# Kernel optimization log

Hardware: AMD Instinct MI355X
Metric: run time of the kernel (lower is better)

The kernel has to match this reference:

```python
import jax, jax.numpy as jnp
import numpy as np

B, T, D = 2, 2048, 1024
NH, DH = 16, 64  # inner = NH*DH = D
SCALE_INIT = 0.02


def setup_inputs() -> dict:
    key = jax.random.key(0)
    kx, kq, kk, kv, ko = jax.random.split(key, 5)
    return {
        "x": jax.random.normal(kx, (B, T, D), dtype=jnp.float32),
        "Wq": jax.random.normal(kq, (D, NH * DH), dtype=jnp.float32) * SCALE_INIT,
        "Wk": jax.random.normal(kk, (D, NH * DH), dtype=jnp.float32) * SCALE_INIT,
        "Wv": jax.random.normal(kv, (D, NH * DH), dtype=jnp.float32) * SCALE_INIT,
        "Wo": jax.random.normal(ko, (NH * DH, D), dtype=jnp.float32) * SCALE_INIT,
    }


def reference(x, Wq, Wk, Wv, Wo):
    # x: (B, T, D)
    b, t, _ = x.shape

    def split_heads(h):
        # (B, T, NH*DH) -> (B, NH, T, DH)
        return h.reshape(b, t, NH, DH).transpose(0, 2, 1, 3)

    q = split_heads(x @ Wq)
    k = split_heads(x @ Wk)
    v = split_heads(x @ Wv)

    scale = jnp.asarray(1.0 / np.sqrt(DH), dtype=x.dtype)
    # The per-chunk loop in the original is mathematically equivalent to
    # full causal attention: each query row attends to keys with k_pos <= q_pos.
    scores = jnp.einsum("bhqd,bhkd->bhqk", q, k) * scale  # (B, NH, T, T)
    causal_mask = jnp.arange(t)[None, :] > jnp.arange(t)[:, None]  # k_pos > q_pos
    scores = jnp.where(causal_mask, -jnp.inf, scores)
    attn = jax.nn.softmax(scores, axis=-1)
    attn = jnp.nan_to_num(attn)  # matches torch.nan_to_num (no fully-masked rows in causal case)
    o = jnp.einsum("bhqk,bhkd->bhqd", attn, v)  # (B, NH, T, DH)
    o = o.transpose(0, 2, 1, 3).reshape(b, t, NH * DH)  # merge heads
    return o @ Wo  # (B, T, D)
```

## Files before the change

### kernel.cpp

```cpp
#include <hip/hip_runtime.h>

#define Bsz 2
#define Tsz 2048
#define Dsz 1024
#define NHsz 16
#define Msz (Bsz*Tsz)

typedef unsigned short bfu;
typedef __attribute__((ext_vector_type(8))) short short8;
typedef __attribute__((ext_vector_type(4))) short short4v;
typedef __attribute__((ext_vector_type(4))) float floatx4;

__device__ __forceinline__ bfu f2bf(float f) {
  unsigned int u = __builtin_bit_cast(unsigned int, f);
  u += 0x7fffu + ((u >> 16) & 1u);
  return (bfu)(u >> 16);
}

__device__ __forceinline__ void async16(const void* g, void* l) {
  void* gnc = (void*)g;
  __builtin_amdgcn_global_load_lds((__attribute__((address_space(1))) void*)gnc,
                                   (__attribute__((address_space(3))) void*)l,
                                   16, 0, 0);
}

__global__ __launch_bounds__(256) void convert_x(const float* __restrict__ x,
                                                 bfu* __restrict__ xb) {
  int i = blockIdx.x * 256 + threadIdx.x;
  float4 v = ((const float4*)x)[i];
  short4v o;
  o[0] = (short)f2bf(v.x); o[1] = (short)f2bf(v.y);
  o[2] = (short)f2bf(v.z); o[3] = (short)f2bf(v.w);
  *(short4v*)(xb + (size_t)i * 4) = o;
}

__global__ __launch_bounds__(256) void transpose_w(const float* __restrict__ W0, const float* __restrict__ W1,
                                                   const float* __restrict__ W2, const float* __restrict__ W3,
                                                   bfu* __restrict__ wt) {
  __shared__ float tile[32][33];
  const float* W = blockIdx.z == 0 ? W0 : blockIdx.z == 1 ? W1 : blockIdx.z == 2 ? W2 : W3;
  bfu* WT = wt + (size_t)blockIdx.z * Dsz * Dsz;
  int tx = threadIdx.x, ty = threadIdx.y;
  int kb = blockIdx.y * 32, nb = blockIdx.x * 32;
#pragma unroll
  for (int i = 0; i < 4; ++i)
    tile[ty + i*8][tx] = W[(size_t)(kb + ty + i*8) * Dsz + nb + tx];
  __syncthreads();
#pragma unroll
  for (int i = 0; i < 4; ++i)
    WT[(size_t)(nb + ty + i*8) * Dsz + kb + tx] = f2bf(tile[tx][ty + i*8]);
}

template <bool F32OUT>
__global__ __launch_bounds__(256) void gemm128(const bfu* __restrict__ A, const bfu* __restrict__ Bt0,
                                               void* __restrict__ C0, int K, int N,
                                               size_t strideB, size_t strideC, float scale0) {
  const int tid = threadIdx.x, wave = tid >> 6, lane = tid & 63;
  const int g = lane >> 4, c = lane & 15;
  const int m0 = blockIdx.y * 128, n0 = blockIdx.x * 128;
  const bfu* Bt = Bt0 + strideB * blockIdx.z;
  const float scale = (blockIdx.z == 0) ? scale0 : 1.0f;
  __shared__ bfu As[128 * 32];
  __shared__ bfu Bs[128 * 32];
  floatx4 acc[4][4] = {};
  const int srow = lane >> 2, scol = (lane & 3) * 8;
  const bfu* gA = A  + (size_t)(m0 + srow) * K + scol;
  const bfu* gB = Bt + (size_t)(n0 + srow) * K + scol;
  const int wm = (wave >> 1) * 64, wn = (wave & 1) * 64;
  for (int k0 = 0; k0 < K; k0 += 32) {
    __syncthreads();
#pragma unroll
    for (int cc = 0; cc < 2; ++cc) {
      const int chunk = wave * 2 + cc;
      async16(gA + (size_t)chunk * 16 * K + k0, &As[chunk * 512]);
      async16(gB + (size_t)chunk * 16 * K + k0, &Bs[chunk * 512]);
    }
    __syncthreads();
    short8 afr[4], bfr[4];
#pragma unroll
    for (int t = 0; t < 4; ++t) afr[t] = *(const short8*)&As[(wm + t*16 + c) * 32 + g * 8];
#pragma unroll
    for (int t = 0; t < 4; ++t) bfr[t] = *(const short8*)&Bs[(wn + t*16 + c) * 32 + g * 8];
#pragma unroll
    for (int i = 0; i < 4; ++i)
#pragma unroll
      for (int j = 0; j < 4; ++j)
        acc[i][j] = __builtin_amdgcn_mfma_f32_16x16x32_bf16(afr[i], bfr[j], acc[i][j], 0, 0, 0);
  }
  const bool vtrans = (!F32OUT) && (blockIdx.z == 2);
#pragma unroll
  for (int i = 0; i < 4; ++i) {
#pragma unroll
    for (int j = 0; j < 4; ++j) {
      const int m = m0 + wm + i*16 + g*4;
      const int n = n0 + wn + j*16 + c;
      if (vtrans) {
        bfu* vtp = (bfu*)C0 + (size_t)2 * strideC;
        size_t o = ((size_t)((m >> 11) * 16 + (n >> 6)) * 64 + (n & 63)) * Tsz + (m & 2047);
        short4v pk;
#pragma unroll
        for (int r = 0; r < 4; ++r) pk[r] = (short)f2bf(acc[i][j][r]);
        *(short4v*)&vtp[o] = pk;
      } else {
#pragma unroll
        for (int r = 0; r < 4; ++r) {
          float v = acc[i][j][r] * scale;
          if (F32OUT) ((float*)C0)[(size_t)(m + r) * N + n] = v;
          else        ((bfu*)C0)[strideC * blockIdx.z + (size_t)(m + r) * N + n] = f2bf(v);
        }
      }
    }
  }
}

__global__ __launch_bounds__(256, 2) void attn_kernel(const bfu* __restrict__ qkv,
                                                      bfu* __restrict__ obuf) {
  const int tid = threadIdx.x, wave = tid >> 6, lane = tid & 63;
  const int g = (lane >> 4) & 3, c = lane & 15, c7 = c & 7;
  const int bh = blockIdx.y, b = bh >> 4, h = bh & 15;
  const size_t hb = (size_t)b * Tsz * Dsz + h * 64;
  const bfu* Qp = qkv + hb;
  const bfu* Kp = qkv + (size_t)Msz * Dsz + hb;
  const bfu* Vt = qkv + (size_t)2 * Msz * Dsz + (size_t)bh * 64 * Tsz;

  __shared__ bfu Ks[128 * 64];
  __shared__ bfu Vs[64 * 128];
  __shared__ bfu Ps[4][16 * 128];

  const int kst_row = lane >> 3;
  const int kst_off = ((lane & 7) ^ kst_row) << 3;
  const int vst_row = lane >> 4;

  for (int half = 0; half < 2; ++half) {
    const int j = half ? (31 - (int)blockIdx.x) : (int)blockIdx.x;
    const int qw = j * 64 + wave * 16;
    const int ktm = j >> 1;

    short8 bq[2];
#pragma unroll
    for (int kk = 0; kk < 2; ++kk)
      bq[kk] = *(const short8*)(Qp + (size_t)(qw + c) * Dsz + kk * 32 + g * 8);

    floatx4 acc[4] = {};
    float mi = -3.0e38f, li = 0.0f;

    for (int kt = 0; kt <= ktm; ++kt) {
      __syncthreads();
#pragma unroll
      for (int cc = 0; cc < 4; ++cc) {
        const int ch = wave * 4 + cc;
        async16(Kp + (size_t)(kt * 128 + ch * 8 + kst_row) * Dsz + kst_off, &Ks[ch * 512]);
        const int drow = ch * 4 + vst_row;
        async16(Vt + (size_t)drow * Tsz + kt * 128 + (((lane & 15) ^ (drow & 7)) << 3), &Vs[ch * 512]);
      }
      __syncthreads();

      floatx4 st[8] = {};
#pragma unroll
      for (int kk = 0; kk < 2; ++kk)
#pragma unroll
        for (int mk = 0; mk < 8; ++mk) {
          const short8 kf = *(const short8*)&Ks[(mk * 16 + c) * 64 + (((kk * 4 + g) ^ c7) << 3)];
          st[mk] = __builtin_amdgcn_mfma_f32_16x16x32_bf16(kf, bq[kk], st[mk], 0, 0, 0);
        }

      if (kt == ktm) {
#pragma unroll
        for (int mk = 0; mk < 8; ++mk) {
          const int keyb = kt * 128 + mk * 16 + g * 4;
#pragma unroll
          for (int r = 0; r < 4; ++r)
            if (keyb + r > qw + c) st[mk][r] = -1.0e38f;
        }
      }

      float mloc = -3.0e38f;
#pragma unroll
      for (int mk = 0; mk < 8; ++mk)
#pragma unroll
        for (int r = 0; r < 4; ++r) mloc = fmaxf(mloc, st[mk][r]);
      mloc = fmaxf(mloc, __shfl_xor(mloc, 16));
      mloc = fmaxf(mloc, __shfl_xor(mloc, 32));
      const float mnew = fmaxf(mi, mloc);
      const float alpha = exp2f(mi - mnew);
      mi = mnew;
      float sum = 0.0f;
#pragma unroll
      for (int mk = 0; mk < 8; ++mk) {
        short4v pk;
#pragma unroll
        for (int r = 0; r < 4; ++r) {
          const float p = exp2f(st[mk][r] - mnew);
          sum += p;
          pk[r] = (short)f2bf(p);
        }
        *(short4v*)&Ps[wave][c * 128 + (((mk * 2 + (g >> 1)) ^ c7) << 3) + ((g & 1) << 2)] = pk;
      }
      sum += __shfl_xor(sum, 16);
      sum += __shfl_xor(sum, 32);
      li = li * alpha + sum;

      float al[4];
#pragma unroll
      for (int r = 0; r < 4; ++r) al[r] = __shfl(alpha, (lane & 48) | (g * 4 + r));
#pragma unroll
      for (int nd = 0; nd < 4; ++nd)
#pragma unroll
        for (int r = 0; r < 4; ++r) acc[nd][r] *= al[r];

#pragma unroll
      for (int kc = 0; kc < 4; ++kc) {
        const int sl = ((kc * 4 + g) ^ c7) << 3;
        const short8 pf = *(const short8*)&Ps[wave][c * 128 + sl];
#pragma unroll
        for (int nd = 0; nd < 4; ++nd) {
          const short8 vf = *(const short8*)&Vs[(nd * 16 + c) * 128 + sl];
          acc[nd] = __builtin_amdgcn_mfma_f32_16x16x32_bf16(pf, vf, acc[nd], 0, 0, 0);
        }
      }
    }

    float inv[4];
#pragma unroll
    for (int r = 0; r < 4; ++r) inv[r] = 1.0f / __shfl(li, (lane & 48) | (g * 4 + r));
#pragma unroll
    for (int nd = 0; nd < 4; ++nd)
#pragma unroll
      for (int r = 0; r < 4; ++r)
        obuf[(size_t)(b * Tsz + qw + g * 4 + r) * Dsz + h * 64 + nd * 16 + c] =
            f2bf(acc[nd][r] * inv[r]);
  }
}

extern "C" void kernel_launch(void* const* d_in, const int* in_sizes, int n_in,
                              void* d_out, int out_size, void* d_ws, size_t ws_size,
                              hipStream_t stream) {
  const float* x  = (const float*)d_in[0];
  const float* Wq = (const float*)d_in[1];
  const float* Wk = (const float*)d_in[2];
  const float* Wv = (const float*)d_in[3];
  const float* Wo = (const float*)d_in[4];
  float* out = (float*)d_out;

  bfu* xb   = (bfu*)d_ws;
  bfu* wt   = xb  + (size_t)Msz * Dsz;
  bfu* qkv  = wt  + (size_t)4 * Dsz * Dsz;
  bfu* obuf = qkv + (size_t)3 * Msz * Dsz;

  convert_x<<<dim3(Msz * Dsz / (256 * 4)), dim3(256), 0, stream>>>(x, xb);
  transpose_w<<<dim3(32, 32, 4), dim3(32, 8), 0, stream>>>(Wq, Wk, Wv, Wo, wt);
  gemm128<false><<<dim3(Dsz / 128, Msz / 128, 3), dim3(256), 0, stream>>>(
      xb, wt, (void*)qkv, Dsz, Dsz, (size_t)Dsz * Dsz, (size_t)Msz * Dsz,
      0.125f * 1.44269504088896f);
  attn_kernel<<<dim3(16, Bsz * NHsz), dim3(256), 0, stream>>>(qkv, obuf);
  gemm128<true><<<dim3(Dsz / 128, Msz / 128, 1), dim3(256), 0, stream>>>(
      obuf, wt + (size_t)3 * Dsz * Dsz, (void*)out, Dsz, Dsz, (size_t)0, (size_t)0, 1.0f);
}
```

Before: 206.4 us.

## Fuse x conversion into QKV GEMM and register-prefetch attention K/V tiles

Removes the separate convert_x kernel: the QKV GEMM now reads fp32 x directly, converts it to bf16 in registers and prefetches the next A tile while computing. The attention kernel swaps its async global-to-LDS K/V loads for register prefetch of the next tile, stored to LDS at the top of each iteration. bf16 packing now uses the HIP intrinsic conversions in place of manual rounding. Together these drop one launch and the xb round trip and aim to overlap loads with compute. The cost is more register pressure and double fp32 A traffic, since the three z-slices each re-read x.

Result: slower. 210.9 us (+2.1%).

```diff
diff --git a/kernel.cpp b/kernel.cpp
--- a/kernel.cpp
+++ b/kernel.cpp
@@ -1,4 +1,6 @@
 #include <hip/hip_runtime.h>
+#include <hip/hip_bf16.h>
+#include <string.h>
 
 #define Bsz 2
 #define Tsz 2048
@@ -17,21 +19,31 @@
   return (bfu)(u >> 16);
 }
 
+__device__ __forceinline__ short4v pack4bf(float a, float b, float c_, float d) {
+  __hip_bfloat162 h01 = __float22bfloat162_rn(make_float2(a, b));
+  __hip_bfloat162 h23 = __float22bfloat162_rn(make_float2(c_, d));
+  uint2 uu;
+  memcpy(&uu.x, &h01, 4);
+  memcpy(&uu.y, &h23, 4);
+  return __builtin_bit_cast(short4v, uu);
+}
+
+__device__ __forceinline__ short8 pack8bf(float4 a, float4 b) {
+  __hip_bfloat162 h0 = __float22bfloat162_rn(make_float2(a.x, a.y));
+  __hip_bfloat162 h1 = __float22bfloat162_rn(make_float2(a.z, a.w));
+  __hip_bfloat162 h2 = __float22bfloat162_rn(make_float2(b.x, b.y));
+  __hip_bfloat162 h3 = __float22bfloat162_rn(make_float2(b.z, b.w));
+  uint4 u;
+  memcpy(&u.x, &h0, 4); memcpy(&u.y, &h1, 4);
+  memcpy(&u.z, &h2, 4); memcpy(&u.w, &h3, 4);
+  return __builtin_bit_cast(short8, u);
+}
+
 __device__ __forceinline__ void async16(const void* g, void* l) {
   void* gnc = (void*)g;
   __builtin_amdgcn_global_load_lds((__attribute__((address_space(1))) void*)gnc,
                                    (__attribute__((address_space(3))) void*)l,
                                    16, 0, 0);
-}
-
-__global__ __launch_bounds__(256) void convert_x(const float* __restrict__ x,
-                                                 bfu* __restrict__ xb) {
-  int i = blockIdx.x * 256 + threadIdx.x;
-  float4 v = ((const float4*)x)[i];
-  short4v o;
-  o[0] = (short)f2bf(v.x); o[1] = (short)f2bf(v.y);
-  o[2] = (short)f2bf(v.z); o[3] = (short)f2bf(v.w);
-  *(short4v*)(xb + (size_t)i * 4) = o;
 }
 
 __global__ __launch_bounds__(256) void transpose_w(const float* __restrict__ W0, const float* __restrict__ W1,
@@ -51,8 +63,8 @@
     WT[(size_t)(nb + ty + i*8) * Dsz + kb + tx] = f2bf(tile[tx][ty + i*8]);
 }
 
-template <bool F32OUT>
-__global__ __launch_bounds__(256) void gemm128(const bfu* __restrict__ A, const bfu* __restrict__ Bt0,
+template <bool F32OUT, bool AF32>
+__global__ __launch_bounds__(256) void gemm128(const void* __restrict__ Ain, const bfu* __restrict__ Bt0,
                                                void* __restrict__ C0, int K, int N,
                                                size_t strideB, size_t strideC, float scale0) {
   const int tid = threadIdx.x, wave = tid >> 6, lane = tid & 63;
@@ -64,18 +76,38 @@
   __shared__ bfu Bs[128 * 32];
   floatx4 acc[4][4] = {};
   const int srow = lane >> 2, scol = (lane & 3) * 8;
-  const bfu* gA = A  + (size_t)(m0 + srow) * K + scol;
   const bfu* gB = Bt + (size_t)(n0 + srow) * K + scol;
   const int wm = (wave >> 1) * 64, wn = (wave & 1) * 64;
+
+  short8 areg[2];
+  if (AF32) {
+#pragma unroll
+    for (int cc = 0; cc < 2; ++cc) {
+      const float* pa = (const float*)Ain +
+          (size_t)(m0 + (wave*2 + cc)*16 + srow) * K + scol;
+      areg[cc] = pack8bf(((const float4*)pa)[0], ((const float4*)pa)[1]);
+    }
+  }
+  const bfu* gA = AF32 ? nullptr : (const bfu*)Ain + (size_t)(m0 + srow) * K + scol;
+
   for (int k0 = 0; k0 < K; k0 += 32) {
     __syncthreads();
 #pragma unroll
     for (int cc = 0; cc < 2; ++cc) {
       const int chunk = wave * 2 + cc;
-      async16(gA + (size_t)chunk * 16 * K + k0, &As[chunk * 512]);
+      if (AF32) *(short8*)&As[chunk * 512 + lane * 8] = areg[cc];
+      else      async16(gA + (size_t)chunk * 16 * K + k0, &As[chunk * 512]);
       async16(gB + (size_t)chunk * 16 * K + k0, &Bs[chunk * 512]);
     }
     __syncthreads();
+    if (AF32 && k0 + 32 < K) {
+#pragma unroll
+      for (int cc = 0; cc < 2; ++cc) {
+        const float* pa = (const float*)Ain +
+            (size_t)(m0 + (wave*2 + cc)*16 + srow) * K + (k0 + 32) + scol;
+        areg[cc] = pack8bf(((const float4*)pa)[0], ((const float4*)pa)[1]);
+      }
+    }
     short8 afr[4], bfr[4];
 #pragma unroll
     for (int t = 0; t < 4; ++t) afr[t] = *(const short8*)&As[(wm + t*16 + c) * 32 + g * 8];
@@ -97,10 +129,7 @@
       if (vtrans) {
         bfu* vtp = (bfu*)C0 + (size_t)2 * strideC;
         size_t o = ((size_t)((m >> 11) * 16 + (n >> 6)) * 64 + (n & 63)) * Tsz + (m & 2047);
-        short4v pk;
-#pragma unroll
-        for (int r = 0; r < 4; ++r) pk[r] = (short)f2bf(acc[i][j][r]);
-        *(short4v*)&vtp[o] = pk;
+        *(short4v*)&vtp[o] = pack4bf(acc[i][j][0], acc[i][j][1], acc[i][j][2], acc[i][j][3]);
       } else {
 #pragma unroll
         for (int r = 0; r < 4; ++r) {
@@ -127,9 +156,11 @@
   __shared__ bfu Vs[64 * 128];
   __shared__ bfu Ps[4][16 * 128];
 
-  const int kst_row = lane >> 3;
-  const int kst_off = ((lane & 7) ^ kst_row) << 3;
-  const int vst_row = lane >> 4;
+  const int krow_in = lane >> 3;
+  const int kcol_g  = (((lane & 7) ^ krow_in) << 3);
+  const int kcol_s  = ((lane & 7) << 3);
+  const int vrow_in = lane >> 4;
+  const int vcol_s  = ((lane & 15) << 3);
 
   for (int half = 0; half < 2; ++half) {
     const int j = half ? (31 - (int)blockIdx.x) : (int)blockIdx.x;
@@ -144,16 +175,35 @@
     floatx4 acc[4] = {};
     float mi = -3.0e38f, li = 0.0f;
 
+    short8 kreg[4], vreg[4];
+#pragma unroll
+    for (int cc = 0; cc < 4; ++cc) {
+      const int ch = wave * 4 + cc;
+      kreg[cc] = *(const short8*)(Kp + (size_t)(ch * 8 + krow_in) * Dsz + kcol_g);
+      const int drow = ch * 4 + vrow_in;
+      vreg[cc] = *(const short8*)(Vt + (size_t)drow * Tsz + (((lane & 15) ^ (drow & 7)) << 3));
+    }
+
     for (int kt = 0; kt <= ktm; ++kt) {
       __syncthreads();
 #pragma unroll
       for (int cc = 0; cc < 4; ++cc) {
         const int ch = wave * 4 + cc;
-        async16(Kp + (size_t)(kt * 128 + ch * 8 + kst_row) * Dsz + kst_off, &Ks[ch * 512]);
-        const int drow = ch * 4 + vst_row;
-        async16(Vt + (size_t)drow * Tsz + kt * 128 + (((lane & 15) ^ (drow & 7)) << 3), &Vs[ch * 512]);
+        *(short8*)&Ks[(ch * 8 + krow_in) * 64 + kcol_s] = kreg[cc];
+        const int drow = ch * 4 + vrow_in;
+        *(short8*)&Vs[drow * 128 + vcol_s] = vreg[cc];
       }
       __syncthreads();
+      if (kt < ktm) {
+#pragma unroll
+        for (int cc = 0; cc < 4; ++cc) {
+          const int ch = wave * 4 + cc;
+          kreg[cc] = *(const short8*)(Kp + (size_t)((kt+1)*128 + ch*8 + krow_in) * Dsz + kcol_g);
+          const int drow = ch * 4 + vrow_in;
+          vreg[cc] = *(const short8*)(Vt + (size_t)drow * Tsz + (kt+1)*128 +
+                                      (((lane & 15) ^ (drow & 7)) << 3));
+        }
+      }
 
       floatx4 st[8] = {};
 #pragma unroll
@@ -187,14 +237,11 @@
       float sum = 0.0f;
 #pragma unroll
       for (int mk = 0; mk < 8; ++mk) {
-        short4v pk;
-#pragma unroll
-        for (int r = 0; r < 4; ++r) {
-          const float p = exp2f(st[mk][r] - mnew);
-          sum += p;
-          pk[r] = (short)f2bf(p);
-        }
-        *(short4v*)&Ps[wave][c * 128 + (((mk * 2 + (g >> 1)) ^ c7) << 3) + ((g & 1) << 2)] = pk;
+        float pr[4];
+#pragma unroll
+        for (int r = 0; r < 4; ++r) { pr[r] = exp2f(st[mk][r] - mnew); sum += pr[r]; }
+        *(short4v*)&Ps[wave][c * 128 + (((mk * 2 + (g >> 1)) ^ c7) << 3) + ((g & 1) << 2)] =
+            pack4bf(pr[0], pr[1], pr[2], pr[3]);
       }
       sum += __shfl_xor(sum, 16);
       sum += __shfl_xor(sum, 32);
@@ -242,17 +289,16 @@
   const float* Wo = (const float*)d_in[4];
   float* out = (float*)d_out;
 
-  bfu* xb   = (bfu*)d_ws;
-  bfu* wt   = xb  + (size_t)Msz * Dsz;
+  bfu* wt   = (bfu*)d_ws;
   bfu* qkv  = wt  + (size_t)4 * Dsz * Dsz;
   bfu* obuf = qkv + (size_t)3 * Msz * Dsz;
 
-  convert_x<<<dim3(Msz * Dsz / (256 * 4)), dim3(256), 0, stream>>>(x, xb);
   transpose_w<<<dim3(32, 32, 4), dim3(32, 8), 0, stream>>>(Wq, Wk, Wv, Wo, wt);
-  gemm128<false><<<dim3(Dsz / 128, Msz / 128, 3), dim3(256), 0, stream>>>(
-      xb, wt, (void*)qkv, Dsz, Dsz, (size_t)Dsz * Dsz, (size_t)Msz * Dsz,
+  gemm128<false, true><<<dim3(Dsz / 128, Msz / 128, 3), dim3(256), 0, stream>>>(
+      (const void*)x, wt, (void*)qkv, Dsz, Dsz, (size_t)Dsz * Dsz, (size_t)Msz * Dsz,
       0.125f * 1.44269504088896f);
   attn_kernel<<<dim3(16, Bsz * NHsz), dim3(256), 0, stream>>>(qkv, obuf);
-  gemm128<true><<<dim3(Dsz / 128, Msz / 128, 1), dim3(256), 0, stream>>>(
-      obuf, wt + (size_t)3 * Dsz * Dsz, (void*)out, Dsz, Dsz, (size_t)0, (size_t)0, 1.0f);
-}
+  gemm128<true, false><<<dim3(Dsz / 128, Msz / 128, 1), dim3(256), 0, stream>>>(
+      (const void*)obuf, wt + (size_t)3 * Dsz * Dsz, (void*)out, Dsz, Dsz,
+      (size_t)0, (size_t)0, 1.0f);
+}
```
